# Kernel tuning notes

Hardware: AMD Instinct MI355X
Metric: run time of the kernel (lower is better)

## Reference

```python
import jax, jax.numpy as jnp
import numpy as np

HEAD_NUM = 8
LN_EPS = 1e-8
NEG_BIG = -1e9

B, T, H = 8, 1024, 2048


def setup_inputs() -> dict:
    key = jax.random.key(0)
    k1, k2, k3, k4 = jax.random.split(key, 4)
    inputs = jax.random.normal(k1, (B, T, H), dtype=jnp.float32)
    # padding mask: 1 marks padded (masked) key positions, like attn_mask()
    valid_len = jax.random.randint(k2, (B, 1), 1, T + 1)
    mask = (jnp.arange(T)[None, :] >= valid_len).astype(jnp.int32)  # [B, T]
    scale = (2.0 ** 0.5) * ((3.0 / H) ** 0.5)
    qkv_w = jax.random.uniform(k3, (H, 3 * H), dtype=jnp.float32) * scale
    o_w = jax.random.uniform(k4, (H, H), dtype=jnp.float32) * scale
    ln_weight = jnp.ones((H,), dtype=jnp.float32)
    ln_bias = jnp.zeros((H,), dtype=jnp.float32)
    return {"inputs": inputs, "mask": mask, "ln_weight": ln_weight,
            "ln_bias": ln_bias, "qkv_w": qkv_w, "o_w": o_w, "isPre": 1}


def reference(inputs, mask, ln_weight, ln_bias, qkv_w, o_w, isPre):
    b, t, h = inputs.shape
    nh = HEAD_NUM
    dh = h // nh
    # LayerNorm (eps=1e-8)
    mu = jnp.mean(inputs, axis=-1, keepdims=True)
    var = jnp.mean((inputs - mu) ** 2, axis=-1, keepdims=True)
    x = (inputs - mu) * jax.lax.rsqrt(var + LN_EPS) * ln_weight + ln_bias
    # QKV projection: Linear with weight = qkv.permute(1,0) => x @ qkv_w
    qkv = x @ qkv_w  # [b, t, 3h]
    qkv = qkv.reshape(b, t, 3, nh, dh).transpose(2, 0, 3, 1, 4)  # [3, b, nh, t, dh]
    q, k, v = qkv[0], qkv[1], qkv[2]
    scores = jnp.einsum('bhqd,bhkd->bhqk', q, k)  # [b, nh, t, t]
    # padding mask over key dim, broadcast over heads and queries
    m = mask[:, None, None, :].astype(jnp.bool_)  # [b,1,1,t]
    if isPre:
        causal = jnp.triu(jnp.ones((t, t), dtype=jnp.bool_), k=1)
        m = m | causal[None, None, :, :]
    # faithful to source: masked_fill with -1e9, THEN scale, then softmax
    scores = jnp.where(m, NEG_BIG, scores) / np.sqrt(dh).astype(np.float32)
    attn = jax.nn.softmax(scores, axis=-1)
    ctx = jnp.einsum('bhqk,bhkd->bhqd', attn, v)  # [b, nh, t, dh]
    ctx = ctx.transpose(0, 2, 1, 3).reshape(b, t, h)
    out = ctx @ o_w + inputs
    return out
```

## Files before the change

### kernel.cpp

```cpp
#include <hip/hip_runtime.h>
#include <cstdint>
#include <cstddef>

typedef __attribute__((ext_vector_type(8))) short s16x8;
typedef __attribute__((ext_vector_type(8))) _Float16 f16x8;
typedef __attribute__((ext_vector_type(4))) float f32x4;

__device__ __forceinline__ unsigned short f2h(float f) {
  union { _Float16 h; unsigned short u; } x;
  x.h = (_Float16)f;
  return x.u;
}

__device__ __forceinline__ f16x8 ldh8(const unsigned short* p) {
  union { s16x8 s; f16x8 h; } u;
  u.s = *(const s16x8*)p;
  return u.h;
}

#define GLD_LDS16(g, l)                                                        \
  __builtin_amdgcn_global_load_lds(                                            \
      (const __attribute__((address_space(1))) void*)(g),                      \
      (__attribute__((address_space(3))) void*)(l), 16, 0, 0)

__global__ __launch_bounds__(256) void ln_kernel(
    const float* __restrict__ x, const float* __restrict__ gw,
    const float* __restrict__ gb, unsigned short* __restrict__ y) {
  const int row = blockIdx.x;
  const int t = threadIdx.x;
  const int w = t >> 6, l = t & 63;
  const float* xr = x + (size_t)row * 2048 + t * 8;
  float4 a = *(const float4*)xr;
  float4 c = *(const float4*)(xr + 4);
  float s = a.x + a.y + a.z + a.w + c.x + c.y + c.z + c.w;
  float q = a.x * a.x + a.y * a.y + a.z * a.z + a.w * a.w +
            c.x * c.x + c.y * c.y + c.z * c.z + c.w * c.w;
#pragma unroll
  for (int off = 1; off < 64; off <<= 1) {
    s += __shfl_xor(s, off);
    q += __shfl_xor(q, off);
  }
  __shared__ float red[8];
  if (l == 0) { red[w] = s; red[4 + w] = q; }
  __syncthreads();
  s = red[0] + red[1] + red[2] + red[3];
  q = red[4] + red[5] + red[6] + red[7];
  const float mu = s * (1.0f / 2048.0f);
  const float var = q * (1.0f / 2048.0f) - mu * mu;
  const float rs = rsqrtf(var + 1e-8f);
  float4 w0 = *(const float4*)(gw + t * 8);
  float4 w1 = *(const float4*)(gw + t * 8 + 4);
  float4 b0 = *(const float4*)(gb + t * 8);
  float4 b1 = *(const float4*)(gb + t * 8 + 4);
  s16x8 ov;
  ov[0] = (short)f2h((a.x - mu) * rs * w0.x + b0.x);
  ov[1] = (short)f2h((a.y - mu) * rs * w0.y + b0.y);
  ov[2] = (short)f2h((a.z - mu) * rs * w0.z + b0.z);
  ov[3] = (short)f2h((a.w - mu) * rs * w0.w + b0.w);
  ov[4] = (short)f2h((c.x - mu) * rs * w1.x + b1.x);
  ov[5] = (short)f2h((c.y - mu) * rs * w1.y + b1.y);
  ov[6] = (short)f2h((c.z - mu) * rs * w1.z + b1.z);
  ov[7] = (short)f2h((c.w - mu) * rs * w1.w + b1.w);
  *(s16x8*)(y + (size_t)row * 2048 + t * 8) = ov;
}

__global__ __launch_bounds__(256) void transpose_w_kernel(
    const float* __restrict__ in, unsigned short* __restrict__ out,
    int R, int C) {
  __shared__ float tile[32][33];
  const int c0 = blockIdx.x * 32, r0 = blockIdx.y * 32;
  const int x = threadIdx.x, y = threadIdx.y;
#pragma unroll
  for (int k = 0; k < 4; ++k)
    tile[y + k * 8][x] = in[(size_t)(r0 + y + k * 8) * C + c0 + x];
  __syncthreads();
#pragma unroll
  for (int k = 0; k < 4; ++k)
    out[(size_t)(c0 + y + k * 8) * R + r0 + x] = f2h(tile[x][y + k * 8]);
}

__global__ __launch_bounds__(256) void transpose_v_kernel(
    const unsigned short* __restrict__ in, unsigned short* __restrict__ out) {
  __shared__ unsigned short tile[32][33];
  const int bh = blockIdx.z;
  const int d0 = blockIdx.x * 32, t0 = blockIdx.y * 32;
  const unsigned short* ip = in + (size_t)bh * 1024 * 256;
  unsigned short* op = out + (size_t)bh * 256 * 1024;
  const int x = threadIdx.x, y = threadIdx.y;
#pragma unroll
  for (int k = 0; k < 4; ++k)
    tile[y + k * 8][x] = ip[(size_t)(t0 + y + k * 8) * 256 + d0 + x];
  __syncthreads();
#pragma unroll
  for (int k = 0; k < 4; ++k)
    op[(size_t)(d0 + y + k * 8) * 1024 + t0 + x] = tile[x][y + k * 8];
}

__device__ __forceinline__ void stage128x32(const unsigned short* gbase, int ldg,
                                            unsigned short* lds, int w, int l) {
#pragma unroll
  for (int i = 0; i < 2; ++i) {
    const int r = (i * 4 + w) * 16 + (l >> 2);
    const int slot = (l & 3) ^ ((l >> 3) & 3);
    const unsigned short* src = gbase + (size_t)r * ldg + slot * 8;
    GLD_LDS16(src, lds + (i * 4 + w) * 512);
  }
}

template <int MODE>
__global__ __launch_bounds__(256, 2) void gemm_bt_kernel(
    const unsigned short* __restrict__ A, const unsigned short* __restrict__ Bt,
    const int K, const int NB,
    unsigned short* __restrict__ qb, unsigned short* __restrict__ kb,
    unsigned short* __restrict__ vb,
    const float* __restrict__ resid, float* __restrict__ outp) {
  __shared__ __align__(16) unsigned short lds_a[128 * 32];
  __shared__ __align__(16) unsigned short lds_b[128 * 32];
  const int tid = threadIdx.x;
  const int w = tid >> 6, l = tid & 63;
  const int flat = blockIdx.x;
  const int cpx = gridDim.x >> 3;
  const int swz = (flat & 7) * cpx + (flat >> 3);
  const int m0 = (swz / NB) * 128, n0 = (swz % NB) * 128;
  const int wm = (w >> 1) * 64, wn = (w & 1) * 64;
  const int lr = l & 15, lg = l >> 4;
  const f32x4 zero = {0.f, 0.f, 0.f, 0.f};
  f32x4 acc[4][4];
#pragma unroll
  for (int m = 0; m < 4; ++m)
#pragma unroll
    for (int n = 0; n < 4; ++n) acc[m][n] = zero;
  const unsigned short* Abase = A + (size_t)m0 * K;
  const unsigned short* Bbase = Bt + (size_t)n0 * K;

  for (int k0 = 0; k0 < K; k0 += 32) {
    __syncthreads();
    stage128x32(Abase + k0, K, lds_a, w, l);
    stage128x32(Bbase + k0, K, lds_b, w, l);
    __syncthreads();
    f16x8 af[4], bfr[4];
#pragma unroll
    for (int m = 0; m < 4; ++m) {
      const int row = wm + m * 16 + lr;
      af[m] = ldh8(&lds_a[row * 32 + ((lg ^ ((row >> 1) & 3)) << 3)]);
    }
#pragma unroll
    for (int n = 0; n < 4; ++n) {
      const int row = wn + n * 16 + lr;
      bfr[n] = ldh8(&lds_b[row * 32 + ((lg ^ ((row >> 1) & 3)) << 3)]);
    }
    __builtin_amdgcn_s_setprio(1);
#pragma unroll
    for (int m = 0; m < 4; ++m)
#pragma unroll
      for (int n = 0; n < 4; ++n)
        acc[m][n] = __builtin_amdgcn_mfma_f32_16x16x32_f16(af[m], bfr[n],
                                                           acc[m][n], 0, 0, 0);
    __builtin_amdgcn_s_setprio(0);
  }

#pragma unroll
  for (int m = 0; m < 4; ++m) {
#pragma unroll
    for (int n = 0; n < 4; ++n) {
      const int gn = n0 + wn + n * 16 + lr;
#pragma unroll
      for (int reg = 0; reg < 4; ++reg) {
        const int gm = m0 + wm + m * 16 + lg * 4 + reg;
        const float v = acc[m][n][reg];
        if constexpr (MODE == 0) {
          const int which = gn >> 11;
          const int head = (gn >> 8) & 7;
          const int d = gn & 255;
          const int b = gm >> 10, t = gm & 1023;
          unsigned short* dst = (which == 0) ? qb : (which == 1) ? kb : vb;
          dst[(((size_t)b * 8 + head) * 1024 + t) * 256 + d] = f2h(v);
        } else {
          outp[(size_t)gm * 2048 + gn] = v + resid[(size_t)gm * 2048 + gn];
        }
      }
    }
  }
}

__global__ __launch_bounds__(512, 2) void attn_kernel(
    const unsigned short* __restrict__ qbuf, const unsigned short* __restrict__ kbuf,
    const unsigned short* __restrict__ vT, const int* __restrict__ mask,
    const int* __restrict__ pre, unsigned short* __restrict__ ctx) {
  __shared__ __align__(16) unsigned short klds[2][32 * 256];
  __shared__ __align__(16) unsigned short vlds[256 * 32];
  __shared__ __align__(16) unsigned short plds[8 * 16 * 32];
  __shared__ int mlds[1024];
  const int tid = threadIdx.x;
  const int w = tid >> 6, l = tid & 63;
  const int lr = l & 15, lg = l >> 4;
  const int j = blockIdx.x;
  const int swz = (j & 7) * 64 + (j >> 3);
  const int bh = swz >> 3, qb = swz & 7;
  const int b = bh >> 3, h = bh & 7;
  const int isPre = pre[0];
  const int qrow0 = qb * 128 + w * 16;

  const unsigned short* kbh = kbuf + (size_t)bh * 1024 * 256;
  const unsigned short* vbh = vT + (size_t)bh * 256 * 1024;
  unsigned short* pl = plds + w * 512;

  *(int2*)&mlds[tid * 2] = *(const int2*)&mask[b * 1024 + tid * 2];

  const unsigned short* qrow =
      qbuf + ((size_t)bh * 1024 + qrow0 + lr) * 256 + lg * 8;
  f16x8 qf[8];
#pragma unroll
  for (int kk = 0; kk < 8; ++kk) qf[kk] = ldh8(qrow + kk * 32);

  const int krow_in = l >> 5;
  const int ksp = l & 31;
  const int vrow_in = l >> 2;
  const int vsp = l & 3;

#pragma unroll
  for (int ii = 0; ii < 2; ++ii) {
    const int i = w * 2 + ii;
    const int kr = i * 2 + krow_in;
    const unsigned short* ksrc =
        kbh + (size_t)kr * 256 + (((ksp ^ (kr & 7))) << 3);
    GLD_LDS16(ksrc, &klds[0][i * 512]);
  }
  __syncthreads();

  const f32x4 zero = {0.f, 0.f, 0.f, 0.f};
  f32x4 oacc[16];
#pragma unroll
  for (int dt = 0; dt < 16; ++dt) oacc[dt] = zero;
  float mrow[4] = {-1e30f, -1e30f, -1e30f, -1e30f};
  float lrow[4] = {0.f, 0.f, 0.f, 0.f};

  for (int t = 0; t < 32; ++t) {
    const int kv0 = t * 32;
#pragma unroll
    for (int ii = 0; ii < 2; ++ii) {
      const int i = w * 2 + ii;
      const int dr = i * 16 + vrow_in;
      const unsigned short* vsrc =
          vbh + (size_t)dr * 1024 + kv0 + ((vsp ^ ((dr >> 1) & 3)) << 3);
      GLD_LDS16(vsrc, &vlds[i * 512]);
    }
    __builtin_amdgcn_sched_barrier(0);
    {
      const int kvn = ((t + 1) & 31) * 32;
#pragma unroll
      for (int ii = 0; ii < 2; ++ii) {
        const int i = w * 2 + ii;
        const int kr = i * 2 + krow_in;
        const unsigned short* ksrc =
            kbh + (size_t)(kvn + kr) * 256 + ((ksp ^ (kr & 7)) << 3);
        GLD_LDS16(ksrc, &klds[(t + 1) & 1][i * 512]);
      }
    }
    __builtin_amdgcn_sched_barrier(0);

    const unsigned short* kcur = klds[t & 1];
    f32x4 sacc[2];
    sacc[0] = zero; sacc[1] = zero;
    __builtin_amdgcn_s_setprio(1);
#pragma unroll
    for (int kk = 0; kk < 8; ++kk) {
#pragma unroll
      for (int n = 0; n < 2; ++n) {
        const int row = n * 16 + lr;
        const f16x8 kf =
            ldh8(&kcur[row * 256 + (((kk * 4 + lg) ^ (row & 7)) << 3)]);
        sacc[n] = __builtin_amdgcn_mfma_f32_16x16x32_f16(qf[kk], kf, sacc[n], 0, 0, 0);
      }
    }
    __builtin_amdgcn_s_setprio(0);

    int mv[2];
    mv[0] = mlds[kv0 + lr];
    mv[1] = mlds[kv0 + 16 + lr];
    float sf[4];
#pragma unroll
    for (int reg = 0; reg < 4; ++reg) {
      const int qg = qrow0 + lg * 4 + reg;
      float mx = -3.0e38f;
#pragma unroll
      for (int n = 0; n < 2; ++n) {
        const int kvg = kv0 + n * 16 + lr;
        float s = sacc[n][reg];
        const bool msk = (mv[n] != 0) || (isPre && (kvg > qg));
        s = msk ? -1e9f : s;
        s *= 0.0625f;
        sacc[n][reg] = s;
        mx = fmaxf(mx, s);
      }
      mx = fmaxf(mx, __shfl_xor(mx, 1));
      mx = fmaxf(mx, __shfl_xor(mx, 2));
      mx = fmaxf(mx, __shfl_xor(mx, 4));
      mx = fmaxf(mx, __shfl_xor(mx, 8));
      const float mnew = fmaxf(mrow[reg], mx);
      sf[reg] = __expf(mrow[reg] - mnew);
      float ps = 0.f;
#pragma unroll
      for (int n = 0; n < 2; ++n) {
        const float pv = __expf(sacc[n][reg] - mnew);
        sacc[n][reg] = pv;
        ps += pv;
      }
      ps += __shfl_xor(ps, 1);
      ps += __shfl_xor(ps, 2);
      ps += __shfl_xor(ps, 4);
      ps += __shfl_xor(ps, 8);
      lrow[reg] = lrow[reg] * sf[reg] + ps;
      mrow[reg] = mnew;
    }
#pragma unroll
    for (int dt = 0; dt < 16; ++dt) {
      f32x4 o = oacc[dt];
      o[0] *= sf[0]; o[1] *= sf[1]; o[2] *= sf[2]; o[3] *= sf[3];
      oacc[dt] = o;
    }

#pragma unroll
    for (int n = 0; n < 2; ++n) {
#pragma unroll
      for (int reg = 0; reg < 4; ++reg) {
        const int row = lg * 4 + reg;
        const int col = n * 16 + lr;
        const int slot = col >> 3;
        pl[row * 32 + (((slot ^ ((row >> 1) & 3)) << 3) | (col & 7))] =
            f2h(sacc[n][reg]);
      }
    }
    asm volatile("s_waitcnt lgkmcnt(0)" ::: "memory");
    __builtin_amdgcn_sched_barrier(0);
    asm volatile("s_waitcnt vmcnt(4)" ::: "memory");
    __builtin_amdgcn_sched_barrier(0);

    const f16x8 pf = ldh8(&pl[lr * 32 + ((lg ^ ((lr >> 1) & 3)) << 3)]);
    __builtin_amdgcn_s_setprio(1);
#pragma unroll
    for (int dt = 0; dt < 16; ++dt) {
      const int row = dt * 16 + lr;
      const f16x8 vf = ldh8(&vlds[row * 32 + ((lg ^ ((row >> 1) & 3)) << 3)]);
      oacc[dt] = __builtin_amdgcn_mfma_f32_16x16x32_f16(pf, vf, oacc[dt], 0, 0, 0);
    }
    __builtin_amdgcn_s_setprio(0);
    __syncthreads();
  }

  float inv[4];
#pragma unroll
  for (int reg = 0; reg < 4; ++reg) inv[reg] = 1.0f / lrow[reg];
#pragma unroll
  for (int dt = 0; dt < 16; ++dt) {
#pragma unroll
    for (int reg = 0; reg < 4; ++reg) {
      const int qg = qrow0 + lg * 4 + reg;
      ctx[((size_t)b * 1024 + qg) * 2048 + h * 256 + dt * 16 + lr] =
          f2h(oacc[dt][reg] * inv[reg]);
    }
  }
}

extern "C" void kernel_launch(void* const* d_in, const int* in_sizes, int n_in,
                              void* d_out, int out_size, void* d_ws,
                              size_t ws_size, hipStream_t stream) {
  const float* x_in = (const float*)d_in[0];
  const int* mask = (const int*)d_in[1];
  const float* lnw = (const float*)d_in[2];
  const float* lnb = (const float*)d_in[3];
  const float* qkvw = (const float*)d_in[4];
  const float* ow = (const float*)d_in[5];
  const int* ispre = (const int*)d_in[6];
  float* out = (float*)d_out;
  char* ws = (char*)d_ws;

  const size_t SZ = 33554432;
  unsigned short* xln = (unsigned short*)(ws);
  unsigned short* wTq = (unsigned short*)(ws + SZ);
  unsigned short* oT = (unsigned short*)(ws + SZ + 25165824);
  unsigned short* qb;
  unsigned short* kb;
  unsigned short* vb;
  const size_t base = SZ + 25165824 + 8388608;
  if (ws_size >= base + 3 * SZ) {
    qb = (unsigned short*)(ws + base);
    kb = (unsigned short*)(ws + base + SZ);
    vb = (unsigned short*)(ws + base + 2 * SZ);
  } else {
    qb = (unsigned short*)d_out;
    kb = qb + SZ / 2;
    vb = (unsigned short*)(ws + base);
  }
  unsigned short* vT = xln;
  unsigned short* ctxb = vb;

  ln_kernel<<<8192, 256, 0, stream>>>(x_in, lnw, lnb, xln);
  transpose_w_kernel<<<dim3(192, 64), dim3(32, 8), 0, stream>>>(qkvw, wTq, 2048, 6144);
  transpose_w_kernel<<<dim3(64, 64), dim3(32, 8), 0, stream>>>(ow, oT, 2048, 2048);
  gemm_bt_kernel<0><<<3072, 256, 0, stream>>>(
      xln, wTq, 2048, 48, qb, kb, vb, nullptr, nullptr);
  transpose_v_kernel<<<dim3(8, 32, 64), dim3(32, 8), 0, stream>>>(vb, vT);
  attn_kernel<<<512, 512, 0, stream>>>(qb, kb, vT, mask, ispre, ctxb);
  gemm_bt_kernel<1><<<1024, 256, 0, stream>>>(
      ctxb, oT, 2048, 16, nullptr, nullptr, nullptr, x_in, out);
}
```

Baseline: 725.5 us.

## Replace 128x128 GEMM with double-buffered 256x256 tile, 8-wave pipelined kernel

Both projection GEMMs move from a 128x128 tile, 4-wave kernel with a synchronous load-then-compute loop to a 256x256 tile, 8-wave kernel. The new kernel double-buffers 64-deep K slices in LDS and issues async global-to-LDS loads for the next slice between MFMA phases, using explicit vmcnt and lgkmcnt waits and barriers. The goal is to hide global load latency behind MFMA work and to double operand reuse per byte loaded. In exchange it uses far more LDS (128KB per block) and more accumulator registers, and the output-projection GEMM now launches only 256 blocks, which may leave the GPU under-filled.

```diff
diff --git a/kernel.cpp b/kernel.cpp
--- a/kernel.cpp
+++ b/kernel.cpp
@@ -96,77 +96,154 @@
     op[(size_t)(d0 + y + k * 8) * 1024 + t0 + x] = tile[x][y + k * 8];
 }
 
-__device__ __forceinline__ void stage128x32(const unsigned short* gbase, int ldg,
-                                            unsigned short* lds, int w, int l) {
+__device__ __forceinline__ void stage256x32(const unsigned short* gbase_k, int ldg,
+                                            unsigned short* region, int w, int l) {
 #pragma unroll
   for (int i = 0; i < 2; ++i) {
-    const int r = (i * 4 + w) * 16 + (l >> 2);
-    const int slot = (l & 3) ^ ((l >> 3) & 3);
-    const unsigned short* src = gbase + (size_t)r * ldg + slot * 8;
-    GLD_LDS16(src, lds + (i * 4 + w) * 512);
-  }
-}
+    const int chunk = w * 2 + i;
+    const int r = chunk * 16 + (l >> 2);
+    const unsigned short* src =
+        gbase_k + (size_t)r * ldg + (((l & 3) ^ ((l >> 3) & 3)) << 3);
+    GLD_LDS16(src, region + chunk * 512);
+  }
+}
+
+#define LGKM0_SB                                                \
+  asm volatile("s_waitcnt lgkmcnt(0)" ::: "memory");            \
+  __builtin_amdgcn_sched_barrier(0)
 
 template <int MODE>
-__global__ __launch_bounds__(256, 2) void gemm_bt_kernel(
+__global__ __launch_bounds__(512, 2) void gemm256_kernel(
     const unsigned short* __restrict__ A, const unsigned short* __restrict__ Bt,
     const int K, const int NB,
     unsigned short* __restrict__ qb, unsigned short* __restrict__ kb,
     unsigned short* __restrict__ vb,
     const float* __restrict__ resid, float* __restrict__ outp) {
-  __shared__ __align__(16) unsigned short lds_a[128 * 32];
-  __shared__ __align__(16) unsigned short lds_b[128 * 32];
+  __shared__ __align__(16) unsigned short ldsA[2][2][256 * 32];
+  __shared__ __align__(16) unsigned short ldsB[2][2][256 * 32];
   const int tid = threadIdx.x;
   const int w = tid >> 6, l = tid & 63;
+  const int lr = l & 15, lg = l >> 4;
+  const int wm = w >> 2, wn = w & 3;
   const int flat = blockIdx.x;
   const int cpx = gridDim.x >> 3;
   const int swz = (flat & 7) * cpx + (flat >> 3);
-  const int m0 = (swz / NB) * 128, n0 = (swz % NB) * 128;
-  const int wm = (w >> 1) * 64, wn = (w & 1) * 64;
-  const int lr = l & 15, lg = l >> 4;
-  const f32x4 zero = {0.f, 0.f, 0.f, 0.f};
-  f32x4 acc[4][4];
-#pragma unroll
-  for (int m = 0; m < 4; ++m)
-#pragma unroll
-    for (int n = 0; n < 4; ++n) acc[m][n] = zero;
+  const int m0 = (swz / NB) * 256, n0 = (swz % NB) * 256;
   const unsigned short* Abase = A + (size_t)m0 * K;
   const unsigned short* Bbase = Bt + (size_t)n0 * K;
 
-  for (int k0 = 0; k0 < K; k0 += 32) {
-    __syncthreads();
-    stage128x32(Abase + k0, K, lds_a, w, l);
-    stage128x32(Bbase + k0, K, lds_b, w, l);
-    __syncthreads();
-    f16x8 af[4], bfr[4];
-#pragma unroll
-    for (int m = 0; m < 4; ++m) {
-      const int row = wm + m * 16 + lr;
-      af[m] = ldh8(&lds_a[row * 32 + ((lg ^ ((row >> 1) & 3)) << 3)]);
-    }
+  const f32x4 zero = {0.f, 0.f, 0.f, 0.f};
+  f32x4 acc[8][4];
+#pragma unroll
+  for (int m = 0; m < 8; ++m)
+#pragma unroll
+    for (int n = 0; n < 4; ++n) acc[m][n] = zero;
+
+  stage256x32(Abase, K, &ldsA[0][0][0], w, l);
+  stage256x32(Bbase, K, &ldsB[0][0][0], w, l);
+  stage256x32(Abase + 32, K, &ldsA[0][1][0], w, l);
+  stage256x32(Bbase + 32, K, &ldsB[0][1][0], w, l);
+  asm volatile("s_waitcnt vmcnt(4)" ::: "memory");
+  __builtin_amdgcn_s_barrier();
+
+  const int NT = K >> 6;
+  for (int t = 0; t < NT; ++t) {
+    const int cur = t & 1, nxt = cur ^ 1;
+    const int ktn = (t + 1 < NT) ? ((t + 1) << 6) : 0;
+    f16x8 af[8], b0, b1;
+    {
+      const unsigned short* Ar = &ldsA[cur][0][0];
+      const unsigned short* Br = &ldsB[cur][0][0];
+#pragma unroll
+      for (int m = 0; m < 8; ++m) {
+        const int R = wm * 128 + m * 16 + lr;
+        af[m] = ldh8(&Ar[R * 32 + ((lg ^ ((R >> 1) & 3)) << 3)]);
+      }
+      { const int R = wn * 64 + lr;      b0 = ldh8(&Br[R * 32 + ((lg ^ ((R >> 1) & 3)) << 3)]); }
+      { const int R = wn * 64 + 16 + lr; b1 = ldh8(&Br[R * 32 + ((lg ^ ((R >> 1) & 3)) << 3)]); }
+      stage256x32(Abase + ktn, K, &ldsA[nxt][0][0], w, l);
+      __builtin_amdgcn_s_barrier();
+      LGKM0_SB;
+      __builtin_amdgcn_s_setprio(1);
+#pragma unroll
+      for (int m = 0; m < 8; ++m) {
+        acc[m][0] = __builtin_amdgcn_mfma_f32_16x16x32_f16(af[m], b0, acc[m][0], 0, 0, 0);
+        acc[m][1] = __builtin_amdgcn_mfma_f32_16x16x32_f16(af[m], b1, acc[m][1], 0, 0, 0);
+      }
+      __builtin_amdgcn_s_setprio(0);
+      __builtin_amdgcn_sched_barrier(0);
+      __builtin_amdgcn_s_barrier();
+    }
+    {
+      const unsigned short* Br = &ldsB[cur][0][0];
+      { const int R = wn * 64 + 32 + lr; b0 = ldh8(&Br[R * 32 + ((lg ^ ((R >> 1) & 3)) << 3)]); }
+      { const int R = wn * 64 + 48 + lr; b1 = ldh8(&Br[R * 32 + ((lg ^ ((R >> 1) & 3)) << 3)]); }
+      stage256x32(Bbase + ktn, K, &ldsB[nxt][0][0], w, l);
+      __builtin_amdgcn_s_barrier();
+      LGKM0_SB;
+      __builtin_amdgcn_s_setprio(1);
+#pragma unroll
+      for (int m = 0; m < 8; ++m) {
+        acc[m][2] = __builtin_amdgcn_mfma_f32_16x16x32_f16(af[m], b0, acc[m][2], 0, 0, 0);
+        acc[m][3] = __builtin_amdgcn_mfma_f32_16x16x32_f16(af[m], b1, acc[m][3], 0, 0, 0);
+      }
+      __builtin_amdgcn_s_setprio(0);
+      __builtin_amdgcn_sched_barrier(0);
+      asm volatile("s_waitcnt vmcnt(4)" ::: "memory");
+      __builtin_amdgcn_s_barrier();
+    }
+    {
+      const unsigned short* Ar = &ldsA[cur][1][0];
+      const unsigned short* Br = &ldsB[cur][1][0];
+#pragma unroll
+      for (int m = 0; m < 8; ++m) {
+        const int R = wm * 128 + m * 16 + lr;
+        af[m] = ldh8(&Ar[R * 32 + ((lg ^ ((R >> 1) & 3)) << 3)]);
+      }
+      { const int R = wn * 64 + lr;      b0 = ldh8(&Br[R * 32 + ((lg ^ ((R >> 1) & 3)) << 3)]); }
+      { const int R = wn * 64 + 16 + lr; b1 = ldh8(&Br[R * 32 + ((lg ^ ((R >> 1) & 3)) << 3)]); }
+      stage256x32(Abase + ktn + 32, K, &ldsA[nxt][1][0], w, l);
+      __builtin_amdgcn_s_barrier();
+      LGKM0_SB;
+      __builtin_amdgcn_s_setprio(1);
+#pragma unroll
+      for (int m = 0; m < 8; ++m) {
+        acc[m][0] = __builtin_amdgcn_mfma_f32_16x16x32_f16(af[m], b0, acc[m][0], 0, 0, 0);
+        acc[m][1] = __builtin_amdgcn_mfma_f32_16x16x32_f16(af[m], b1, acc[m][1], 0, 0, 0);
+      }
+      __builtin_amdgcn_s_setprio(0);
+      __builtin_amdgcn_sched_barrier(0);
+      __builtin_amdgcn_s_barrier();
+    }
+    {
+      const unsigned short* Br = &ldsB[cur][1][0];
+      { const int R = wn * 64 + 32 + lr; b0 = ldh8(&Br[R * 32 + ((lg ^ ((R >> 1) & 3)) << 3)]); }
+      { const int R = wn * 64 + 48 + lr; b1 = ldh8(&Br[R * 32 + ((lg ^ ((R >> 1) & 3)) << 3)]); }
+      stage256x32(Bbase + ktn + 32, K, &ldsB[nxt][1][0], w, l);
+      __builtin_amdgcn_s_barrier();
+      LGKM0_SB;
+      __builtin_amdgcn_s_setprio(1);
+#pragma unroll
+      for (int m = 0; m < 8; ++m) {
+        acc[m][2] = __builtin_amdgcn_mfma_f32_16x16x32_f16(af[m], b0, acc[m][2], 0, 0, 0);
+        acc[m][3] = __builtin_amdgcn_mfma_f32_16x16x32_f16(af[m], b1, acc[m][3], 0, 0, 0);
+      }
+      __builtin_amdgcn_s_setprio(0);
+      __builtin_amdgcn_sched_barrier(0);
+      asm volatile("s_waitcnt vmcnt(4)" ::: "memory");
+      __builtin_amdgcn_s_barrier();
+    }
+  }
+  asm volatile("s_waitcnt vmcnt(0)" ::: "memory");
+
+#pragma unroll
+  for (int m = 0; m < 8; ++m) {
 #pragma unroll
     for (int n = 0; n < 4; ++n) {
-      const int row = wn + n * 16 + lr;
-      bfr[n] = ldh8(&lds_b[row * 32 + ((lg ^ ((row >> 1) & 3)) << 3)]);
-    }
-    __builtin_amdgcn_s_setprio(1);
-#pragma unroll
-    for (int m = 0; m < 4; ++m)
-#pragma unroll
-      for (int n = 0; n < 4; ++n)
-        acc[m][n] = __builtin_amdgcn_mfma_f32_16x16x32_f16(af[m], bfr[n],
-                                                           acc[m][n], 0, 0, 0);
-    __builtin_amdgcn_s_setprio(0);
-  }
-
-#pragma unroll
-  for (int m = 0; m < 4; ++m) {
-#pragma unroll
-    for (int n = 0; n < 4; ++n) {
-      const int gn = n0 + wn + n * 16 + lr;
+      const int gn = n0 + wn * 64 + n * 16 + lr;
 #pragma unroll
       for (int reg = 0; reg < 4; ++reg) {
-        const int gm = m0 + wm + m * 16 + lg * 4 + reg;
+        const int gm = m0 + wm * 128 + m * 16 + lg * 4 + reg;
         const float v = acc[m][n][reg];
         if constexpr (MODE == 0) {
           const int which = gn >> 11;
@@ -398,10 +475,10 @@
   ln_kernel<<<8192, 256, 0, stream>>>(x_in, lnw, lnb, xln);
   transpose_w_kernel<<<dim3(192, 64), dim3(32, 8), 0, stream>>>(qkvw, wTq, 2048, 6144);
   transpose_w_kernel<<<dim3(64, 64), dim3(32, 8), 0, stream>>>(ow, oT, 2048, 2048);
-  gemm_bt_kernel<0><<<3072, 256, 0, stream>>>(
-      xln, wTq, 2048, 48, qb, kb, vb, nullptr, nullptr);
+  gemm256_kernel<0><<<768, 512, 0, stream>>>(
+      xln, wTq, 2048, 24, qb, kb, vb, nullptr, nullptr);
   transpose_v_kernel<<<dim3(8, 32, 64), dim3(32, 8), 0, stream>>>(vb, vT);
   attn_kernel<<<512, 512, 0, stream>>>(qb, kb, vT, mask, ispre, ctxb);
-  gemm_bt_kernel<1><<<1024, 256, 0, stream>>>(
-      ctxb, oT, 2048, 16, nullptr, nullptr, nullptr, x_in, out);
-}
+  gemm256_kernel<1><<<256, 512, 0, stream>>>(
+      ctxb, oT, 2048, 8, nullptr, nullptr, nullptr, x_in, out);
+}
```

Result: faster. 656.0 us (-9.6%).
